# Kernel tuning notes

Measured on AMD Instinct MI355X. Metric: run time of the kernel, lower is better.

Reference implementation:

```python
import jax, jax.numpy as jnp
import numpy as np

EPS = 1e-3  # freq_scaling_eps default

def _mean_transf(mu, sigma, w, p):
    return jnp.exp(-0.5 * (sigma * w) ** 2) * jnp.sin(p + mu * w)

def _var_transf(mu, sigma, w, p):
    return 0.5 - 0.5 * jnp.exp(-2 * (sigma * w) ** 2) * jnp.cos(2 * (p + mu * w)) - _mean_transf(mu, sigma, w, p) ** 2

def setup_inputs() -> dict:
    key = jax.random.key(0)
    k1, k2, k3, k4 = jax.random.split(key, 4)
    B, IN, F, OUT = 8192, 512, 64, 512
    x = jax.random.normal(k1, (B, IN), dtype=jnp.float32)
    freqs = jax.random.normal(k2, (1, 1, F), dtype=jnp.float32)  # normal(stddev=1.0) init
    phases = jnp.zeros((1, 1, F), dtype=jnp.float32)             # zeros init
    # variance_scaling(1.0,'fan_in',uniform): limit = sqrt(3/fan_in)
    lim_b = np.sqrt(3.0 / F)
    beta = jax.random.uniform(k3, (F, OUT), dtype=jnp.float32, minval=-lim_b, maxval=lim_b)
    lim_l = np.sqrt(3.0 / IN)
    lamb = jax.random.uniform(k4, (IN, OUT), dtype=jnp.float32, minval=-lim_l, maxval=lim_l)
    bias = jnp.zeros((OUT,), dtype=jnp.float32)
    return {"x": x, "freqs": freqs, "phases": phases, "beta": beta, "lamb": lamb, "bias": bias}

def reference(x, freqs, phases, beta, lamb, bias):
    # x: [B, I]; freqs/phases: [1, 1, F]; beta: [F, O]; lamb: [I, O]; bias: [O]
    xb = jnp.sin(freqs * x[:, :, None] + phases)  # [B, I, F]
    mean = _mean_transf(0.0, 1.0, freqs, phases)  # [1, 1, F]
    var = _var_transf(0.0, 1.0, freqs, phases)    # [1, 1, F]
    xb = (xb - mean) / jnp.sqrt(EPS + var)
    out = jnp.einsum('bif,fo,io->bo', xb, beta, lamb)  # bilinear contraction
    return out + bias
```

## Files before the change

kernel.cpp:

```cpp
#include <hip/hip_runtime.h>
#include <hip/hip_bf16.h>


#define TB 256

typedef __attribute__((ext_vector_type(8))) short short8;
typedef __attribute__((ext_vector_type(4))) float floatx4;
typedef __attribute__((ext_vector_type(4))) unsigned int uintx4;
typedef __attribute__((ext_vector_type(4))) unsigned short ushort4t;

__device__ __forceinline__ unsigned pk_bf16(float a, float b) {
    union { float f; unsigned u; } ca, cb;
    ca.f = a; cb.f = b;
    unsigned ua = ca.u + 0x8000u;
    unsigned ub = cb.u + 0x8000u;
    return __builtin_amdgcn_perm(ub, ua, 0x07060302u);
}
__device__ __forceinline__ unsigned short f_to_bf16u(float v) {
    union { __hip_bfloat16 h; unsigned short u; } cv;
    cv.h = __float2bfloat16(v);
    return cv.u;
}
__device__ __forceinline__ float bf16u_to_f(unsigned short v) {
    union { unsigned u; float f; } cv; cv.u = ((unsigned)v) << 16; return cv.f;
}

__device__ __forceinline__ short8 sin_frag8(const float xv[8], float wfr, float pfr) {
    float s[8];
    #pragma unroll
    for (int j = 0; j < 8; ++j) {
        float t = fmaf(xv[j], wfr, pfr);
        float u = t - __builtin_rintf(t);
        s[j] = __builtin_amdgcn_sinf(u);
    }
    union { uintx4 u; short8 h; } cv;
    cv.u.x = pk_bf16(s[0], s[1]); cv.u.y = pk_bf16(s[2], s[3]);
    cv.u.z = pk_bf16(s[4], s[5]); cv.u.w = pk_bf16(s[6], s[7]);
    return cv.h;
}

__global__ __launch_bounds__(TB, 2)
void actlayer_kernel(const float* __restrict__ x,
                     const float* __restrict__ freqs,
                     const float* __restrict__ phases,
                     const float* __restrict__ beta,
                     const float* __restrict__ lamb,
                     const float* __restrict__ bias,
                     float* __restrict__ out)
{
    constexpr int I = 512, F = 64, O = 512;
    constexpr int BN = 128;
    const int t  = threadIdx.x;
    const int bx = blockIdx.x;
    const int bn = bx & 3;
    const int bm = bx >> 2;
    const int n0 = bn * BN;
    const int m0 = bm * 64;

    __shared__ __align__(16) unsigned short L_sh[BN][72];
    __shared__ __align__(16) unsigned short brP_sh[F][16][12];
    __shared__ float wrev_sh[F], prev_sh[F], r_sh[F], m_sh[F];
    __shared__ float c_sh[BN];
    __shared__ float slp_sh[2][BN];

    if (t < F) {
        float wq = freqs[t];
        float ph = phases[t];
        float e1 = expf(-0.5f * wq * wq);
        float mean = e1 * sinf(ph);
        float e2 = expf(-2.0f * wq * wq);
        float var = 0.5f - 0.5f * e2 * cosf(2.0f * ph) - mean * mean;
        float r = 1.0f / sqrtf(1e-3f + var);
        wrev_sh[t] = wq * 0.15915494309189535f;
        prev_sh[t] = ph * 0.15915494309189535f;
        r_sh[t] = r;
        m_sh[t] = mean;
    }
    {
        int n = t & 127, half = t >> 7;
        float s = 0.f;
        const float* lp = lamb + (size_t)(half * 256) * O + n0 + n;
        #pragma unroll 8
        for (int i = 0; i < 256; ++i) s += lp[(size_t)i * O];
        slp_sh[half][n] = s;
    }
    __syncthreads();
    #pragma unroll
    for (int j = 0; j < 32; ++j) {
        int e = t + TB * j;
        int f = e >> 7;
        int rem = e & 127;
        int w = rem >> 4;
        int c = rem & 15;
        float bv = beta[f * O + n0 + w * 16 + c] * r_sh[f];
        brP_sh[f][c][w] = f_to_bf16u(bv);
    }
    __syncthreads();
    if (t < BN) {
        int c = t & 15, w = t >> 4;
        float sb = 0.f;
        #pragma unroll
        for (int f = 0; f < F; ++f) sb += bf16u_to_f(brP_sh[f][c][w]) * m_sh[f];
        c_sh[t] = bias[n0 + t] - sb * (slp_sh[0][t] + slp_sh[1][t]);
    }

    const int lane = t & 63;
    const int wid  = t >> 6;
    const int l15  = lane & 15;
    const int quad = lane >> 4;
    const int row  = m0 + wid * 16 + l15;

    floatx4 oacc[8];
    #pragma unroll
    for (int nt = 0; nt < 8; ++nt) oacc[nt] = (floatx4){0.f, 0.f, 0.f, 0.f};
    const floatx4 zero4 = (floatx4){0.f, 0.f, 0.f, 0.f};

    #pragma unroll 1
    for (int it = 0; it < 8; ++it) {
        const int i0 = it * 64;
        {
            int n  = t & 127;
            int kh = t >> 7;
            const float* lp = lamb + (size_t)(i0 + kh * 32) * O + n0 + n;
            float v[32];
            #pragma unroll
            for (int k = 0; k < 32; ++k) v[k] = lp[(size_t)k * O];
            #pragma unroll
            for (int rr = 0; rr < 4; ++rr) {
                uintx4 w4;
                w4.x = pk_bf16(v[rr*8+0], v[rr*8+1]);
                w4.y = pk_bf16(v[rr*8+2], v[rr*8+3]);
                w4.z = pk_bf16(v[rr*8+4], v[rr*8+5]);
                w4.w = pk_bf16(v[rr*8+6], v[rr*8+7]);
                *(uintx4*)&L_sh[n][kh * 32 + rr * 8] = w4;
            }
        }
        float xr0[8], xr1[8];
        {
            const float* xp = x + (size_t)row * I + i0 + quad * 8;
            float4 a0 = *(const float4*)(xp);
            float4 a1 = *(const float4*)(xp + 4);
            float4 b0 = *(const float4*)(xp + 32);
            float4 b1 = *(const float4*)(xp + 36);
            xr0[0]=a0.x; xr0[1]=a0.y; xr0[2]=a0.z; xr0[3]=a0.w;
            xr0[4]=a1.x; xr0[5]=a1.y; xr0[6]=a1.z; xr0[7]=a1.w;
            xr1[0]=b0.x; xr1[1]=b0.y; xr1[2]=b0.z; xr1[3]=b0.w;
            xr1[4]=b1.x; xr1[5]=b1.y; xr1[6]=b1.z; xr1[7]=b1.w;
        }
        short8 afA0 = sin_frag8(xr0, wrev_sh[0], prev_sh[0]);
        short8 afA1 = sin_frag8(xr1, wrev_sh[0], prev_sh[0]);
        short8 afB0 = sin_frag8(xr0, wrev_sh[1], prev_sh[1]);
        short8 afB1 = sin_frag8(xr1, wrev_sh[1], prev_sh[1]);
        __syncthreads();
        short8 lf[2][8];
        #pragma unroll
        for (int kk = 0; kk < 2; ++kk)
            #pragma unroll
            for (int nt = 0; nt < 8; ++nt)
                lf[kk][nt] = *(const short8*)&L_sh[nt*16 + l15][kk*32 + quad*8];

        ushort4t bruA0 = *(const ushort4t*)&brP_sh[0][l15][0];
        ushort4t bruA1 = *(const ushort4t*)&brP_sh[0][l15][4];
        ushort4t bruB0 = *(const ushort4t*)&brP_sh[1][l15][0];
        ushort4t bruB1 = *(const ushort4t*)&brP_sh[1][l15][4];

        #pragma unroll 1
        for (int f = 0; f < F; f += 2) {
            float brA[8], brB[8];
            #pragma unroll
            for (int q = 0; q < 4; ++q) {
                brA[q]     = bf16u_to_f(bruA0[q]);
                brA[4 + q] = bf16u_to_f(bruA1[q]);
                brB[q]     = bf16u_to_f(bruB0[q]);
                brB[4 + q] = bf16u_to_f(bruB1[q]);
            }
            short8 nfA0 = afA0, nfA1 = afA1, nfB0 = afB0, nfB1 = afB1;
            if (f + 2 < F) {
                bruA0 = *(const ushort4t*)&brP_sh[f + 2][l15][0];
                bruA1 = *(const ushort4t*)&brP_sh[f + 2][l15][4];
                bruB0 = *(const ushort4t*)&brP_sh[f + 3][l15][0];
                bruB1 = *(const ushort4t*)&brP_sh[f + 3][l15][4];
                float wA = wrev_sh[f + 2], pA = prev_sh[f + 2];
                float wB = wrev_sh[f + 3], pB = prev_sh[f + 3];
                nfA0 = sin_frag8(xr0, wA, pA);
                nfA1 = sin_frag8(xr1, wA, pA);
                nfB0 = sin_frag8(xr0, wB, pB);
                nfB1 = sin_frag8(xr1, wB, pB);
            }
            #pragma unroll
            for (int nt = 0; nt < 8; ++nt) {
                floatx4 s = __builtin_amdgcn_mfma_f32_16x16x32_bf16(
                    afA0, lf[0][nt], zero4, 0, 0, 0);
                s = __builtin_amdgcn_mfma_f32_16x16x32_bf16(
                    afA1, lf[1][nt], s, 0, 0, 0);
                oacc[nt] += brA[nt] * s;
            }
            #pragma unroll
            for (int nt = 0; nt < 8; ++nt) {
                floatx4 s = __builtin_amdgcn_mfma_f32_16x16x32_bf16(
                    afB0, lf[0][nt], zero4, 0, 0, 0);
                s = __builtin_amdgcn_mfma_f32_16x16x32_bf16(
                    afB1, lf[1][nt], s, 0, 0, 0);
                oacc[nt] += brB[nt] * s;
            }
            __syncthreads();
            afA0 = nfA0; afA1 = nfA1; afB0 = nfB0; afB1 = nfB1;
        }
    }

    #pragma unroll
    for (int nt = 0; nt < 8; ++nt) {
        int gn = n0 + nt*16 + l15;
        float cv = c_sh[nt*16 + l15];
        int gm = m0 + wid*16 + quad*4;
        #pragma unroll
        for (int rg = 0; rg < 4; ++rg) {
            out[(size_t)(gm + rg) * O + gn] = oacc[nt][rg] + cv;
        }
    }
}

extern "C" void kernel_launch(void* const* d_in, const int* in_sizes, int n_in,
                              void* d_out, int out_size, void* d_ws, size_t ws_size,
                              hipStream_t stream) {
    const float* x      = (const float*)d_in[0];
    const float* freqs  = (const float*)d_in[1];
    const float* phases = (const float*)d_in[2];
    const float* beta   = (const float*)d_in[3];
    const float* lamb   = (const float*)d_in[4];
    const float* bias   = (const float*)d_in[5];
    float* out = (float*)d_out;

    dim3 grid(512);
    dim3 block(TB);
    hipLaunchKernelGGL(actlayer_kernel, grid, block, 0, stream,
                       x, freqs, phases, beta, lamb, bias, out);
}
```

Before: 457.8 us.

## Retile to 32x256 blocks and share sin fragments through LDS double buffer

```diff
diff --git a/kernel.cpp b/kernel.cpp
--- a/kernel.cpp
+++ b/kernel.cpp
@@ -7,7 +7,7 @@
 typedef __attribute__((ext_vector_type(8))) short short8;
 typedef __attribute__((ext_vector_type(4))) float floatx4;
 typedef __attribute__((ext_vector_type(4))) unsigned int uintx4;
-typedef __attribute__((ext_vector_type(4))) unsigned short ushort4t;
+typedef __attribute__((ext_vector_type(8))) unsigned short ushort8t;
 
 __device__ __forceinline__ unsigned pk_bf16(float a, float b) {
     union { float f; unsigned u; } ca, cb;
@@ -25,7 +25,7 @@
     union { unsigned u; float f; } cv; cv.u = ((unsigned)v) << 16; return cv.f;
 }
 
-__device__ __forceinline__ short8 sin_frag8(const float xv[8], float wfr, float pfr) {
+__device__ __forceinline__ uintx4 sin_pack8(const float xv[8], float wfr, float pfr) {
     float s[8];
     #pragma unroll
     for (int j = 0; j < 8; ++j) {
@@ -33,10 +33,10 @@
         float u = t - __builtin_rintf(t);
         s[j] = __builtin_amdgcn_sinf(u);
     }
-    union { uintx4 u; short8 h; } cv;
-    cv.u.x = pk_bf16(s[0], s[1]); cv.u.y = pk_bf16(s[2], s[3]);
-    cv.u.z = pk_bf16(s[4], s[5]); cv.u.w = pk_bf16(s[6], s[7]);
-    return cv.h;
+    uintx4 w4;
+    w4.x = pk_bf16(s[0], s[1]); w4.y = pk_bf16(s[2], s[3]);
+    w4.z = pk_bf16(s[4], s[5]); w4.w = pk_bf16(s[6], s[7]);
+    return w4;
 }
 
 __global__ __launch_bounds__(TB, 2)
@@ -49,19 +49,18 @@
                      float* __restrict__ out)
 {
     constexpr int I = 512, F = 64, O = 512;
-    constexpr int BN = 128;
     const int t  = threadIdx.x;
     const int bx = blockIdx.x;
-    const int bn = bx & 3;
-    const int bm = bx >> 2;
-    const int n0 = bn * BN;
-    const int m0 = bm * 64;
-
-    __shared__ __align__(16) unsigned short L_sh[BN][72];
-    __shared__ __align__(16) unsigned short brP_sh[F][16][12];
+    const int bn = bx & 1;
+    const int bm = bx >> 1;
+    const int n0 = bn * 256;
+    const int m0 = bm * 32;
+
+    __shared__ __align__(16) unsigned short A_sh[2][2][32][72];
+    __shared__ __align__(16) unsigned short L_scr[128][72];
+    __shared__ __align__(16) unsigned short brP_sh[F][16][16];
     __shared__ float wrev_sh[F], prev_sh[F], r_sh[F], m_sh[F];
-    __shared__ float c_sh[BN];
-    __shared__ float slp_sh[2][BN];
+    __shared__ float c_sh[256];
 
     if (t < F) {
         float wq = freqs[t];
@@ -76,39 +75,40 @@
         r_sh[t] = r;
         m_sh[t] = mean;
     }
-    {
-        int n = t & 127, half = t >> 7;
-        float s = 0.f;
-        const float* lp = lamb + (size_t)(half * 256) * O + n0 + n;
-        #pragma unroll 8
-        for (int i = 0; i < 256; ++i) s += lp[(size_t)i * O];
-        slp_sh[half][n] = s;
-    }
     __syncthreads();
     #pragma unroll
-    for (int j = 0; j < 32; ++j) {
+    for (int j = 0; j < 64; ++j) {
         int e = t + TB * j;
-        int f = e >> 7;
-        int rem = e & 127;
+        int f = e >> 8;
+        int rem = e & 255;
         int w = rem >> 4;
         int c = rem & 15;
         float bv = beta[f * O + n0 + w * 16 + c] * r_sh[f];
         brP_sh[f][c][w] = f_to_bf16u(bv);
     }
     __syncthreads();
-    if (t < BN) {
+    {
         int c = t & 15, w = t >> 4;
         float sb = 0.f;
         #pragma unroll
         for (int f = 0; f < F; ++f) sb += bf16u_to_f(brP_sh[f][c][w]) * m_sh[f];
-        c_sh[t] = bias[n0 + t] - sb * (slp_sh[0][t] + slp_sh[1][t]);
+        float sl = 0.f;
+        const float* lp = lamb + n0 + t;
+        #pragma unroll 8
+        for (int i = 0; i < I; ++i) sl += lp[(size_t)i * O];
+        c_sh[t] = bias[n0 + t] - sb * sl;
     }
 
     const int lane = t & 63;
     const int wid  = t >> 6;
+    const int mg   = wid >> 1;
+    const int ng   = wid & 1;
     const int l15  = lane & 15;
     const int quad = lane >> 4;
-    const int row  = m0 + wid * 16 + l15;
+    const int kr = t & 7;
+    const int r0 = t >> 3;
+    const int nL  = t & 127;
+    const int khL = t >> 7;
 
     floatx4 oacc[8];
     #pragma unroll
@@ -119,9 +119,7 @@
     for (int it = 0; it < 8; ++it) {
         const int i0 = it * 64;
         {
-            int n  = t & 127;
-            int kh = t >> 7;
-            const float* lp = lamb + (size_t)(i0 + kh * 32) * O + n0 + n;
+            const float* lp = lamb + (size_t)(i0 + khL * 32) * O + n0 + nL;
             float v[32];
             #pragma unroll
             for (int k = 0; k < 32; ++k) v[k] = lp[(size_t)k * O];
@@ -132,60 +130,73 @@
                 w4.y = pk_bf16(v[rr*8+2], v[rr*8+3]);
                 w4.z = pk_bf16(v[rr*8+4], v[rr*8+5]);
                 w4.w = pk_bf16(v[rr*8+6], v[rr*8+7]);
-                *(uintx4*)&L_sh[n][kh * 32 + rr * 8] = w4;
-            }
-        }
-        float xr0[8], xr1[8];
+                *(uintx4*)&L_scr[nL][khL * 32 + rr * 8] = w4;
+            }
+        }
+        float xs[8];
         {
-            const float* xp = x + (size_t)row * I + i0 + quad * 8;
+            const float* xp = x + (size_t)(m0 + r0) * I + i0 + kr * 8;
             float4 a0 = *(const float4*)(xp);
             float4 a1 = *(const float4*)(xp + 4);
-            float4 b0 = *(const float4*)(xp + 32);
-            float4 b1 = *(const float4*)(xp + 36);
-            xr0[0]=a0.x; xr0[1]=a0.y; xr0[2]=a0.z; xr0[3]=a0.w;
-            xr0[4]=a1.x; xr0[5]=a1.y; xr0[6]=a1.z; xr0[7]=a1.w;
-            xr1[0]=b0.x; xr1[1]=b0.y; xr1[2]=b0.z; xr1[3]=b0.w;
-            xr1[4]=b1.x; xr1[5]=b1.y; xr1[6]=b1.z; xr1[7]=b1.w;
-        }
-        short8 afA0 = sin_frag8(xr0, wrev_sh[0], prev_sh[0]);
-        short8 afA1 = sin_frag8(xr1, wrev_sh[0], prev_sh[0]);
-        short8 afB0 = sin_frag8(xr0, wrev_sh[1], prev_sh[1]);
-        short8 afB1 = sin_frag8(xr1, wrev_sh[1], prev_sh[1]);
+            xs[0]=a0.x; xs[1]=a0.y; xs[2]=a0.z; xs[3]=a0.w;
+            xs[4]=a1.x; xs[5]=a1.y; xs[6]=a1.z; xs[7]=a1.w;
+        }
         __syncthreads();
         short8 lf[2][8];
-        #pragma unroll
-        for (int kk = 0; kk < 2; ++kk)
-            #pragma unroll
-            for (int nt = 0; nt < 8; ++nt)
-                lf[kk][nt] = *(const short8*)&L_sh[nt*16 + l15][kk*32 + quad*8];
-
-        ushort4t bruA0 = *(const ushort4t*)&brP_sh[0][l15][0];
-        ushort4t bruA1 = *(const ushort4t*)&brP_sh[0][l15][4];
-        ushort4t bruB0 = *(const ushort4t*)&brP_sh[1][l15][0];
-        ushort4t bruB1 = *(const ushort4t*)&brP_sh[1][l15][4];
-
+        if (ng == 0) {
+            #pragma unroll
+            for (int kk = 0; kk < 2; ++kk)
+                #pragma unroll
+                for (int nt = 0; nt < 8; ++nt)
+                    lf[kk][nt] = *(const short8*)&L_scr[nt*16 + l15][kk*32 + quad*8];
+        }
+        __syncthreads();
+        {
+            const float* lp = lamb + (size_t)(i0 + khL * 32) * O + n0 + 128 + nL;
+            float v[32];
+            #pragma unroll
+            for (int k = 0; k < 32; ++k) v[k] = lp[(size_t)k * O];
+            #pragma unroll
+            for (int rr = 0; rr < 4; ++rr) {
+                uintx4 w4;
+                w4.x = pk_bf16(v[rr*8+0], v[rr*8+1]);
+                w4.y = pk_bf16(v[rr*8+2], v[rr*8+3]);
+                w4.z = pk_bf16(v[rr*8+4], v[rr*8+5]);
+                w4.w = pk_bf16(v[rr*8+6], v[rr*8+7]);
+                *(uintx4*)&L_scr[nL][khL * 32 + rr * 8] = w4;
+            }
+        }
+        *(uintx4*)&A_sh[0][0][r0][kr * 8] = sin_pack8(xs, wrev_sh[0], prev_sh[0]);
+        *(uintx4*)&A_sh[0][1][r0][kr * 8] = sin_pack8(xs, wrev_sh[1], prev_sh[1]);
+        __syncthreads();
+        if (ng == 1) {
+            #pragma unroll
+            for (int kk = 0; kk < 2; ++kk)
+                #pragma unroll
+                for (int nt = 0; nt < 8; ++nt)
+                    lf[kk][nt] = *(const short8*)&L_scr[nt*16 + l15][kk*32 + quad*8];
+        }
+
+        int cur = 0;
         #pragma unroll 1
         for (int f = 0; f < F; f += 2) {
+            ushort8t bruA = *(const ushort8t*)&brP_sh[f][l15][ng * 8];
+            ushort8t bruB = *(const ushort8t*)&brP_sh[f + 1][l15][ng * 8];
+            const int arow = mg * 16 + l15;
+            short8 afA0 = *(const short8*)&A_sh[cur][0][arow][quad * 8];
+            short8 afA1 = *(const short8*)&A_sh[cur][0][arow][32 + quad * 8];
+            short8 afB0 = *(const short8*)&A_sh[cur][1][arow][quad * 8];
+            short8 afB1 = *(const short8*)&A_sh[cur][1][arow][32 + quad * 8];
             float brA[8], brB[8];
             #pragma unroll
-            for (int q = 0; q < 4; ++q) {
-                brA[q]     = bf16u_to_f(bruA0[q]);
-                brA[4 + q] = bf16u_to_f(bruA1[q]);
-                brB[q]     = bf16u_to_f(bruB0[q]);
-                brB[4 + q] = bf16u_to_f(bruB1[q]);
-            }
-            short8 nfA0 = afA0, nfA1 = afA1, nfB0 = afB0, nfB1 = afB1;
-            if (f + 2 < F) {
-                bruA0 = *(const ushort4t*)&brP_sh[f + 2][l15][0];
-                bruA1 = *(const ushort4t*)&brP_sh[f + 2][l15][4];
-                bruB0 = *(const ushort4t*)&brP_sh[f + 3][l15][0];
-                bruB1 = *(const ushort4t*)&brP_sh[f + 3][l15][4];
-                float wA = wrev_sh[f + 2], pA = prev_sh[f + 2];
-                float wB = wrev_sh[f + 3], pB = prev_sh[f + 3];
-                nfA0 = sin_frag8(xr0, wA, pA);
-                nfA1 = sin_frag8(xr1, wA, pA);
-                nfB0 = sin_frag8(xr0, wB, pB);
-                nfB1 = sin_frag8(xr1, wB, pB);
+            for (int q = 0; q < 8; ++q) {
+                brA[q] = bf16u_to_f(bruA[q]);
+                brB[q] = bf16u_to_f(bruB[q]);
+            }
+            const bool more = (f + 2 < F);
+            if (more) {
+                *(uintx4*)&A_sh[cur ^ 1][0][r0][kr * 8] =
+                    sin_pack8(xs, wrev_sh[f + 2], prev_sh[f + 2]);
             }
             #pragma unroll
             for (int nt = 0; nt < 8; ++nt) {
@@ -195,6 +206,10 @@
                     afA1, lf[1][nt], s, 0, 0, 0);
                 oacc[nt] += brA[nt] * s;
             }
+            if (more) {
+                *(uintx4*)&A_sh[cur ^ 1][1][r0][kr * 8] =
+                    sin_pack8(xs, wrev_sh[f + 3], prev_sh[f + 3]);
+            }
             #pragma unroll
             for (int nt = 0; nt < 8; ++nt) {
                 floatx4 s = __builtin_amdgcn_mfma_f32_16x16x32_bf16(
@@ -204,15 +219,15 @@
                 oacc[nt] += brB[nt] * s;
             }
             __syncthreads();
-            afA0 = nfA0; afA1 = nfA1; afB0 = nfB0; afB1 = nfB1;
+            cur ^= 1;
         }
     }
 
     #pragma unroll
     for (int nt = 0; nt < 8; ++nt) {
-        int gn = n0 + nt*16 + l15;
-        float cv = c_sh[nt*16 + l15];
-        int gm = m0 + wid*16 + quad*4;
+        int gn = n0 + ng * 128 + nt * 16 + l15;
+        float cv = c_sh[ng * 128 + nt * 16 + l15];
+        int gm = m0 + mg * 16 + quad * 4;
         #pragma unroll
         for (int rg = 0; rg < 4; ++rg) {
             out[(size_t)(gm + rg) * O + gn] = oacc[nt][rg] + cv;
```

Result: faster. 404.3 us (-11.7%).
